# Kernel tuning notes

Hardware: AMD Instinct MI355X
Metric: run time of the kernel (lower is better)

## Reference

```python
import jax, jax.numpy as jnp
import numpy as np

N_NODES = 50000
N_EDGES = 800000
NUM_GRAPHS = 64
F_IN, F_HID, F_HID2, F_OUT = 128, 96, 48, 32


def gcn_conv(x, W, b, src, dst, n_nodes):
    # PyG GCNConv: h = x @ W; out = D^{-1/2} (A+I) D^{-1/2} h + b
    # src/dst already include self loops; degree computed on dst.
    h = x @ W  # [N, F_out]
    deg = jax.ops.segment_sum(jnp.ones(dst.shape[0], dtype=h.dtype), dst, num_segments=n_nodes)
    dinv = jax.lax.rsqrt(deg)  # deg >= 1 due to self loops
    norm = dinv[src] * dinv[dst]  # [E]
    msg = h[src] * norm[:, None]  # gather + scale
    out = jax.ops.segment_sum(msg, dst, num_segments=n_nodes)  # scatter-add
    return out + b


def setup_inputs() -> dict:
    key = jax.random.key(0)
    ks = jax.random.split(key, 10)
    x = jax.random.normal(ks[0], (N_NODES, F_IN), dtype=jnp.float32)
    edge_index = jax.random.randint(ks[1], (2, N_EDGES), 0, N_NODES, dtype=jnp.int64)
    batch = jnp.sort(jax.random.randint(ks[2], (N_NODES,), 0, NUM_GRAPHS, dtype=jnp.int64))
    def glorot(k, fi, fo):
        s = np.sqrt(6.0 / (fi + fo)).astype(np.float32)
        return jax.random.uniform(k, (fi, fo), dtype=jnp.float32, minval=-s, maxval=s)
    W1 = glorot(ks[3], F_IN, F_HID)
    b1 = jnp.zeros((F_HID,), dtype=jnp.float32)
    W2 = glorot(ks[4], F_HID, F_HID2)
    b2 = jnp.zeros((F_HID2,), dtype=jnp.float32)
    W3 = glorot(ks[5], F_HID2, F_OUT)
    b3 = jnp.zeros((F_OUT,), dtype=jnp.float32)
    return {"x": x, "edge_index": edge_index, "batch": batch,
            "W1": W1, "b1": b1, "W2": W2, "b2": b2, "W3": W3, "b3": b3}


def reference(x, edge_index, batch, W1, b1, W2, b2, W3, b3):
    n = x.shape[0]
    loops = jnp.arange(n, dtype=edge_index.dtype)
    src = jnp.concatenate([edge_index[0], loops])
    dst = jnp.concatenate([edge_index[1], loops])

    h = jax.nn.relu(gcn_conv(x, W1, b1, src, dst, n))
    h = jax.nn.relu(gcn_conv(h, W2, b2, src, dst, n))
    h = jax.nn.relu(gcn_conv(h, W3, b3, src, dst, n))

    # global mean pool over graphs in the batch
    sums = jax.ops.segment_sum(h, batch, num_segments=NUM_GRAPHS)
    cnt = jax.ops.segment_sum(jnp.ones((n,), dtype=h.dtype), batch, num_segments=NUM_GRAPHS)
    return sums / jnp.maximum(cnt, 1.0)[:, None]
```

## Files before the change

### kernel.cpp

```cpp
#include <hip/hip_runtime.h>

#define N_NODES 50000
#define N_EDGES 800000
#define NUM_GRAPHS 64

#define CAPLOG 6
#define CAP    (1 << CAPLOG)

__device__ __forceinline__ float bf_lo(unsigned u) { return __uint_as_float(u << 16); }
__device__ __forceinline__ float bf_hi(unsigned u) { return __uint_as_float(u & 0xffff0000u); }
__device__ __forceinline__ unsigned short f2bf(float f) {
    unsigned u = __float_as_uint(f);
    return (unsigned short)((u + 0x7fffu + ((u >> 16) & 1u)) >> 16);
}

#define SC_NG    4
#define SC_BPG   256
#define SC_GRID  (SC_NG * SC_BPG)
#define NPG      ((N_NODES + SC_NG - 1) / SC_NG)
__global__ __launch_bounds__(256) void k_scatter_xcd(
        const int* __restrict__ ei, int* __restrict__ cnt,
        unsigned short* __restrict__ csr,
        const int* __restrict__ batch, int* __restrict__ start) {
    if (blockIdx.x == SC_GRID) {
        int t = threadIdx.x;
        if (t <= NUM_GRAPHS) {
            int lo = 0, hi = N_NODES;
            while (lo < hi) {
                int mid = (lo + hi) >> 1;
                if (batch[mid] < t) lo = mid + 1; else hi = mid;
            }
            start[t] = lo;
        }
        return;
    }
    const int g  = blockIdx.x & (SC_NG - 1);
    const int b  = blockIdx.x / SC_NG;
    const int lo = g * NPG, hi = lo + NPG;
    const int* __restrict__ dst = ei + N_EDGES;
    for (int e = b * 256 + threadIdx.x; e < N_EDGES; e += 256 * SC_BPG) {
        int d = dst[e];
        if (d >= lo && d < hi) {
            int old = atomicAdd(&cnt[d], 1);
            if (old < CAP) csr[(d << CAPLOG) + old] = (unsigned short)ei[e];
        }
    }
}

template <int K, int M, int MT, int FTH, int NTH, int NT, int OSTRIDE>
__global__ __launch_bounds__(FTH * NTH)
void k_gemm(const float* __restrict__ X, const float* __restrict__ W,
            const int* __restrict__ cnt, unsigned short* __restrict__ H) {
    constexpr int BLOCK = FTH * NTH;
    __shared__ float ws[K * MT];
    const int tid = threadIdx.x;
    const int n0 = blockIdx.x * (NTH * NT);
    const int c0 = blockIdx.y * MT;

    for (int i = tid; i < K * MT / 4; i += BLOCK) {
        int k = i / (MT / 4), cv = i % (MT / 4);
        *(float4*)&ws[k * MT + cv * 4] = *(const float4*)&W[k * M + c0 + cv * 4];
    }
    __syncthreads();

    const int ft = tid % FTH;
    const int nt = tid / FTH;
    const float* xp[NT];
    #pragma unroll
    for (int i = 0; i < NT; ++i) {
        int node = n0 + nt * NT + i;
        int nc = node < N_NODES ? node : N_NODES - 1;
        xp[i] = X + (size_t)nc * K;
    }
    float acc[NT][4];
    #pragma unroll
    for (int i = 0; i < NT; ++i) { acc[i][0] = acc[i][1] = acc[i][2] = acc[i][3] = 0.f; }

    for (int k = 0; k < K; k += 4) {
        float4 w0 = *(const float4*)&ws[(k + 0) * MT + ft * 4];
        float4 w1 = *(const float4*)&ws[(k + 1) * MT + ft * 4];
        float4 w2 = *(const float4*)&ws[(k + 2) * MT + ft * 4];
        float4 w3 = *(const float4*)&ws[(k + 3) * MT + ft * 4];
        #pragma unroll
        for (int i = 0; i < NT; ++i) {
            float4 xv = *(const float4*)(xp[i] + k);
            acc[i][0] += xv.x * w0.x + xv.y * w1.x + xv.z * w2.x + xv.w * w3.x;
            acc[i][1] += xv.x * w0.y + xv.y * w1.y + xv.z * w2.y + xv.w * w3.y;
            acc[i][2] += xv.x * w0.z + xv.y * w1.z + xv.z * w2.z + xv.w * w3.z;
            acc[i][3] += xv.x * w0.w + xv.y * w1.w + xv.z * w2.w + xv.w * w3.w;
        }
    }
    #pragma unroll
    for (int i = 0; i < NT; ++i) {
        int node = n0 + nt * NT + i;
        if (node < N_NODES) {
            float s = rsqrtf((float)(cnt[node] + 1));
            ushort4 o;
            o.x = f2bf(acc[i][0] * s); o.y = f2bf(acc[i][1] * s);
            o.z = f2bf(acc[i][2] * s); o.w = f2bf(acc[i][3] * s);
            *(ushort4*)&H[(size_t)node * OSTRIDE + c0 + ft * 4] = o;
        }
    }
}

__global__ __launch_bounds__(384) void k_agg12(
        const unsigned short* __restrict__ H1, const int* __restrict__ cnt,
        const unsigned short* __restrict__ csr, const float* __restrict__ b1,
        const float* __restrict__ W2, unsigned short* __restrict__ H2) {
    __shared__ float Ws[96 * 48];
    __shared__ float T[32][97];
    const int t = threadIdx.x;
    for (int i = t; i < 1152; i += 384)
        *(float4*)&Ws[i * 4] = *(const float4*)&W2[i * 4];

    const int n_l = t / 12, c = t % 12;
    const int node = blockIdx.x * 32 + n_l;
    if (node < N_NODES) {
        int deg = cnt[node];
        int e0 = node << CAPLOG;
        int e1 = e0 + min(deg, CAP);
        float d = rsqrtf((float)(deg + 1));
        const unsigned short* Hc = H1 + c * 8;
        uint4 sv = *(const uint4*)(Hc + (size_t)node * 96);
        float a0 = bf_lo(sv.x), a1 = bf_hi(sv.x), a2 = bf_lo(sv.y), a3 = bf_hi(sv.y);
        float a4 = bf_lo(sv.z), a5 = bf_hi(sv.z), a6 = bf_lo(sv.w), a7 = bf_hi(sv.w);
        for (int e = e0; e < e1; ++e) {
            int s = csr[e];
            uint4 v = *(const uint4*)(Hc + (size_t)s * 96);
            a0 += bf_lo(v.x); a1 += bf_hi(v.x);
            a2 += bf_lo(v.y); a3 += bf_hi(v.y);
            a4 += bf_lo(v.z); a5 += bf_hi(v.z);
            a6 += bf_lo(v.w); a7 += bf_hi(v.w);
        }
        const float4* bp = (const float4*)(b1 + c * 8);
        float4 b0 = bp[0], bb1 = bp[1];
        float* Tr = &T[n_l][c * 8];
        Tr[0] = fmaxf(a0 * d + b0.x, 0.f);  Tr[1] = fmaxf(a1 * d + b0.y, 0.f);
        Tr[2] = fmaxf(a2 * d + b0.z, 0.f);  Tr[3] = fmaxf(a3 * d + b0.w, 0.f);
        Tr[4] = fmaxf(a4 * d + bb1.x, 0.f); Tr[5] = fmaxf(a5 * d + bb1.y, 0.f);
        Tr[6] = fmaxf(a6 * d + bb1.z, 0.f); Tr[7] = fmaxf(a7 * d + bb1.w, 0.f);
    }
    __syncthreads();

    const int n2 = t / 12;
    const int f0 = (t % 12) * 4;
    const int gn = blockIdx.x * 32 + n2;
    if (gn < N_NODES) {
        float4 acc = make_float4(0.f, 0.f, 0.f, 0.f);
        for (int k = 0; k < 96; ++k) {
            float tv = T[n2][k];
            float4 wv = *(const float4*)&Ws[k * 48 + f0];
            acc.x += tv * wv.x; acc.y += tv * wv.y; acc.z += tv * wv.z; acc.w += tv * wv.w;
        }
        float s2 = rsqrtf((float)(cnt[gn] + 1));
        ushort4 o;
        o.x = f2bf(acc.x * s2); o.y = f2bf(acc.y * s2);
        o.z = f2bf(acc.z * s2); o.w = f2bf(acc.w * s2);
        *(ushort4*)&H2[(size_t)gn * 64 + f0] = o;
    }
}

__global__ __launch_bounds__(384) void k_agg23(
        const unsigned short* __restrict__ H2, const int* __restrict__ cnt,
        const unsigned short* __restrict__ csr, const float* __restrict__ b2,
        const float* __restrict__ W3, unsigned short* __restrict__ H3) {
    __shared__ float Ws[48 * 32];
    __shared__ float T[64][49];
    const int t = threadIdx.x;
    for (int i = t; i < 384; i += 384)
        *(float4*)&Ws[i * 4] = *(const float4*)&W3[i * 4];

    const int n_l = t / 6, c = t % 6;
    const int node = blockIdx.x * 64 + n_l;
    if (node < N_NODES) {
        int deg = cnt[node];
        int e0 = node << CAPLOG;
        int e1 = e0 + min(deg, CAP);
        float d = rsqrtf((float)(deg + 1));
        const unsigned short* Hc = H2 + c * 8;
        uint4 sv = *(const uint4*)(Hc + (size_t)node * 64);
        float a0 = bf_lo(sv.x), a1 = bf_hi(sv.x), a2 = bf_lo(sv.y), a3 = bf_hi(sv.y);
        float a4 = bf_lo(sv.z), a5 = bf_hi(sv.z), a6 = bf_lo(sv.w), a7 = bf_hi(sv.w);
        for (int e = e0; e < e1; ++e) {
            int s = csr[e];
            uint4 v = *(const uint4*)(Hc + (size_t)s * 64);
            a0 += bf_lo(v.x); a1 += bf_hi(v.x);
            a2 += bf_lo(v.y); a3 += bf_hi(v.y);
            a4 += bf_lo(v.z); a5 += bf_hi(v.z);
            a6 += bf_lo(v.w); a7 += bf_hi(v.w);
        }
        const float4* bp = (const float4*)(b2 + c * 8);
        float4 b0 = bp[0], bb1 = bp[1];
        float* Tr = &T[n_l][c * 8];
        Tr[0] = fmaxf(a0 * d + b0.x, 0.f);  Tr[1] = fmaxf(a1 * d + b0.y, 0.f);
        Tr[2] = fmaxf(a2 * d + b0.z, 0.f);  Tr[3] = fmaxf(a3 * d + b0.w, 0.f);
        Tr[4] = fmaxf(a4 * d + bb1.x, 0.f); Tr[5] = fmaxf(a5 * d + bb1.y, 0.f);
        Tr[6] = fmaxf(a6 * d + bb1.z, 0.f); Tr[7] = fmaxf(a7 * d + bb1.w, 0.f);
    }
    __syncthreads();

    for (int vid = t; vid < 512; vid += 384) {
        const int n2 = vid / 8;
        const int f0 = (vid % 8) * 4;
        const int gn = blockIdx.x * 64 + n2;
        if (gn < N_NODES) {
            float4 acc = make_float4(0.f, 0.f, 0.f, 0.f);
            for (int k = 0; k < 48; ++k) {
                float tv = T[n2][k];
                float4 wv = *(const float4*)&Ws[k * 32 + f0];
                acc.x += tv * wv.x; acc.y += tv * wv.y; acc.z += tv * wv.z; acc.w += tv * wv.w;
            }
            float s3 = rsqrtf((float)(cnt[gn] + 1));
            ushort4 o;
            o.x = f2bf(acc.x * s3); o.y = f2bf(acc.y * s3);
            o.z = f2bf(acc.z * s3); o.w = f2bf(acc.w * s3);
            *(ushort4*)&H3[(size_t)gn * 32 + f0] = o;
        }
    }
}

__global__ __launch_bounds__(256) void k_agg3p(
        const unsigned short* __restrict__ H3, const int* __restrict__ cnt,
        const unsigned short* __restrict__ csr, const float* __restrict__ b3,
        const int* __restrict__ batch, const int* __restrict__ start,
        float* __restrict__ gsum) {
    __shared__ float T[64][33];
    __shared__ float R[8][32];
    const int t = threadIdx.x;
    const int base = blockIdx.x * 64;

    const int n_l = t / 4, c = t % 4;
    const int node = base + n_l;
    if (node < N_NODES) {
        int deg = cnt[node];
        int e0 = node << CAPLOG;
        int e1 = e0 + min(deg, CAP);
        float d = rsqrtf((float)(deg + 1));
        const unsigned short* Hc = H3 + c * 8;
        uint4 sv = *(const uint4*)(Hc + (size_t)node * 32);
        float a0 = bf_lo(sv.x), a1 = bf_hi(sv.x), a2 = bf_lo(sv.y), a3 = bf_hi(sv.y);
        float a4 = bf_lo(sv.z), a5 = bf_hi(sv.z), a6 = bf_lo(sv.w), a7 = bf_hi(sv.w);
        for (int e = e0; e < e1; ++e) {
            int s = csr[e];
            uint4 v = *(const uint4*)(Hc + (size_t)s * 32);
            a0 += bf_lo(v.x); a1 += bf_hi(v.x);
            a2 += bf_lo(v.y); a3 += bf_hi(v.y);
            a4 += bf_lo(v.z); a5 += bf_hi(v.z);
            a6 += bf_lo(v.w); a7 += bf_hi(v.w);
        }
        const float4* bp = (const float4*)(b3 + c * 8);
        float4 b0 = bp[0], b1 = bp[1];
        float* Tr = &T[n_l][c * 8];
        Tr[0] = fmaxf(a0 * d + b0.x, 0.f); Tr[1] = fmaxf(a1 * d + b0.y, 0.f);
        Tr[2] = fmaxf(a2 * d + b0.z, 0.f); Tr[3] = fmaxf(a3 * d + b0.w, 0.f);
        Tr[4] = fmaxf(a4 * d + b1.x, 0.f); Tr[5] = fmaxf(a5 * d + b1.y, 0.f);
        Tr[6] = fmaxf(a6 * d + b1.z, 0.f); Tr[7] = fmaxf(a7 * d + b1.w, 0.f);
    }
    __syncthreads();

    const int g_lo = batch[base < N_NODES ? base : N_NODES - 1];
    const int last = base + 63 < N_NODES ? base + 63 : N_NODES - 1;
    const int g_hi = batch[last];
    const int f = t & 31, k = t >> 5;
    for (int g = g_lo; g <= g_hi; ++g) {
        int r_lo = start[g] - base;     if (r_lo < 0) r_lo = 0;
        int r_hi = start[g + 1] - base; if (r_hi > 64) r_hi = 64;
        float p = 0.f;
        for (int r = r_lo + k; r < r_hi; r += 8) p += T[r][f];
        R[k][f] = p;
        __syncthreads();
        if (k == 0) {
            float s = R[0][f] + R[1][f] + R[2][f] + R[3][f]
                    + R[4][f] + R[5][f] + R[6][f] + R[7][f];
            if (r_hi > r_lo) atomicAdd(&gsum[g * 32 + f], s);
        }
        __syncthreads();
    }
}

__global__ void k_final(const float* __restrict__ gsum, const int* __restrict__ start,
                        float* __restrict__ out) {
    int t = blockIdx.x * blockDim.x + threadIdx.x;
    if (t < NUM_GRAPHS * 32) {
        int g = t >> 5;
        float c = (float)(start[g + 1] - start[g]);
        out[t] = gsum[t] / fmaxf(c, 1.0f);
    }
}

extern "C" void kernel_launch(void* const* d_in, const int* in_sizes, int n_in,
                              void* d_out, int out_size, void* d_ws, size_t ws_size,
                              hipStream_t stream) {
    const float* x     = (const float*)d_in[0];
    const int*   ei    = (const int*)d_in[1];
    const int*   batch = (const int*)d_in[2];
    const float* W1    = (const float*)d_in[3];
    const float* b1    = (const float*)d_in[4];
    const float* W2    = (const float*)d_in[5];
    const float* b2    = (const float*)d_in[6];
    const float* W3    = (const float*)d_in[7];
    const float* b3    = (const float*)d_in[8];
    float* out = (float*)d_out;

    char* ws = (char*)d_ws;
    size_t o = 0;
    auto alloc = [&](size_t bytes) {
        char* p = ws + o;
        o = (o + bytes + 255) & ~(size_t)255;
        return p;
    };
    unsigned short* H1 = (unsigned short*)alloc((size_t)N_NODES * 96 * 2);
    unsigned short* H2 = (unsigned short*)alloc((size_t)N_NODES * 64 * 2);
    unsigned short* H3 = (unsigned short*)alloc((size_t)N_NODES * 32 * 2);
    int*   cnt    = (int*)alloc((size_t)N_NODES * 4);
    unsigned short* csr = (unsigned short*)alloc((size_t)N_NODES * CAP * 2);
    int*   start  = (int*)alloc((NUM_GRAPHS + 1) * 4);
    float* gsum   = (float*)alloc((size_t)NUM_GRAPHS * 32 * 4);

    hipMemsetAsync(cnt, 0, (size_t)N_NODES * 4, stream);
    hipMemsetAsync(gsum, 0, (size_t)NUM_GRAPHS * 32 * 4, stream);

    hipLaunchKernelGGL(k_scatter_xcd, dim3(SC_GRID + 1), dim3(256), 0, stream, ei, cnt, csr, batch, start);
    hipLaunchKernelGGL((k_gemm<128, 96, 48, 12, 16, 4, 96>), dim3((N_NODES + 63) / 64, 2), dim3(192), 0, stream,
                       x, W1, cnt, H1);
    hipLaunchKernelGGL(k_agg12, dim3((N_NODES + 31) / 32), dim3(384), 0, stream,
                       H1, cnt, csr, b1, W2, H2);
    hipLaunchKernelGGL(k_agg23, dim3((N_NODES + 63) / 64), dim3(384), 0, stream,
                       H2, cnt, csr, b2, W3, H3);
    hipLaunchKernelGGL(k_agg3p, dim3((N_NODES + 63) / 64), dim3(256), 0, stream,
                       H3, cnt, csr, b3, batch, start, gsum);
    hipLaunchKernelGGL(k_final, dim3((NUM_GRAPHS * 32 + 255) / 256), dim3(256), 0, stream,
                       gsum, start, out);
}
```

Before: 244.9 us.

## Embed degree counter in CSR row and unroll neighbor gather by four

Stores each node's degree counter in the last two slots of its CSR row, so scatter atomics and later degree reads share one cache line with the neighbor list and the separate cnt array goes away. Neighbor aggregation is factored into a helper that loads four indices as a ushort4 and issues four independent row gathers per iteration. Padding lanes point at a zero row appended to each H buffer. The per-node inverse sqrt degree is also kept in shared memory for the second matmul stage. The trade-offs are a larger memset over the whole CSR buffer and capacity dropping from 64 to 62 neighbors per node.

```diff
diff --git a/kernel.cpp b/kernel.cpp
--- a/kernel.cpp
+++ b/kernel.cpp
@@ -4,8 +4,10 @@
 #define N_EDGES 800000
 #define NUM_GRAPHS 64
 
-#define CAPLOG 6
-#define CAP    (1 << CAPLOG)
+#define CAPLOG   6
+#define CAP      (1 << CAPLOG)
+#define CAPSLOTS 62
+#define ZROW     N_NODES
 
 __device__ __forceinline__ float bf_lo(unsigned u) { return __uint_as_float(u << 16); }
 __device__ __forceinline__ float bf_hi(unsigned u) { return __uint_as_float(u & 0xffff0000u); }
@@ -14,13 +16,45 @@
     return (unsigned short)((u + 0x7fffu + ((u >> 16) & 1u)) >> 16);
 }
 
+__device__ __forceinline__ int ld_deg(const unsigned short* __restrict__ csr, int n) {
+    return *(const int*)(csr + ((size_t)n << CAPLOG) + CAPSLOTS);
+}
+
+template<int S>
+__device__ __forceinline__ void agg_row8(const unsigned short* __restrict__ Hc,
+                                         const unsigned short* __restrict__ csr,
+                                         int node, int m, float a[8]) {
+    uint4 sv = *(const uint4*)(Hc + (size_t)node * S);
+    a[0] = bf_lo(sv.x); a[1] = bf_hi(sv.x); a[2] = bf_lo(sv.y); a[3] = bf_hi(sv.y);
+    a[4] = bf_lo(sv.z); a[5] = bf_hi(sv.z); a[6] = bf_lo(sv.w); a[7] = bf_hi(sv.w);
+    const int e0 = node << CAPLOG, e1 = e0 + m;
+    for (int e = e0; e < e1; e += 4) {
+        ushort4 ss = *(const ushort4*)&csr[e];
+        int s0 = ss.x;
+        int s1 = (e + 1 < e1) ? (int)ss.y : ZROW;
+        int s2 = (e + 2 < e1) ? (int)ss.z : ZROW;
+        int s3 = (e + 3 < e1) ? (int)ss.w : ZROW;
+        uint4 v0 = *(const uint4*)(Hc + (size_t)s0 * S);
+        uint4 v1 = *(const uint4*)(Hc + (size_t)s1 * S);
+        uint4 v2 = *(const uint4*)(Hc + (size_t)s2 * S);
+        uint4 v3 = *(const uint4*)(Hc + (size_t)s3 * S);
+        a[0] += bf_lo(v0.x) + bf_lo(v1.x) + bf_lo(v2.x) + bf_lo(v3.x);
+        a[1] += bf_hi(v0.x) + bf_hi(v1.x) + bf_hi(v2.x) + bf_hi(v3.x);
+        a[2] += bf_lo(v0.y) + bf_lo(v1.y) + bf_lo(v2.y) + bf_lo(v3.y);
+        a[3] += bf_hi(v0.y) + bf_hi(v1.y) + bf_hi(v2.y) + bf_hi(v3.y);
+        a[4] += bf_lo(v0.z) + bf_lo(v1.z) + bf_lo(v2.z) + bf_lo(v3.z);
+        a[5] += bf_hi(v0.z) + bf_hi(v1.z) + bf_hi(v2.z) + bf_hi(v3.z);
+        a[6] += bf_lo(v0.w) + bf_lo(v1.w) + bf_lo(v2.w) + bf_lo(v3.w);
+        a[7] += bf_hi(v0.w) + bf_hi(v1.w) + bf_hi(v2.w) + bf_hi(v3.w);
+    }
+}
+
 #define SC_NG    4
 #define SC_BPG   256
 #define SC_GRID  (SC_NG * SC_BPG)
 #define NPG      ((N_NODES + SC_NG - 1) / SC_NG)
 __global__ __launch_bounds__(256) void k_scatter_xcd(
-        const int* __restrict__ ei, int* __restrict__ cnt,
-        unsigned short* __restrict__ csr,
+        const int* __restrict__ ei, unsigned short* __restrict__ csr,
         const int* __restrict__ batch, int* __restrict__ start) {
     if (blockIdx.x == SC_GRID) {
         int t = threadIdx.x;
@@ -41,8 +75,8 @@
     for (int e = b * 256 + threadIdx.x; e < N_EDGES; e += 256 * SC_BPG) {
         int d = dst[e];
         if (d >= lo && d < hi) {
-            int old = atomicAdd(&cnt[d], 1);
-            if (old < CAP) csr[(d << CAPLOG) + old] = (unsigned short)ei[e];
+            int old = atomicAdd((int*)(csr + ((size_t)d << CAPLOG) + CAPSLOTS), 1);
+            if (old < CAPSLOTS) csr[(d << CAPLOG) + old] = (unsigned short)ei[e];
         }
     }
 }
@@ -50,12 +84,17 @@
 template <int K, int M, int MT, int FTH, int NTH, int NT, int OSTRIDE>
 __global__ __launch_bounds__(FTH * NTH)
 void k_gemm(const float* __restrict__ X, const float* __restrict__ W,
-            const int* __restrict__ cnt, unsigned short* __restrict__ H) {
+            const unsigned short* __restrict__ csr, unsigned short* __restrict__ H) {
     constexpr int BLOCK = FTH * NTH;
     __shared__ float ws[K * MT];
     const int tid = threadIdx.x;
     const int n0 = blockIdx.x * (NTH * NT);
     const int c0 = blockIdx.y * MT;
+
+    if (blockIdx.x == 0 && blockIdx.y == 0 && tid < M / 4) {
+        ushort4 z = make_ushort4(0, 0, 0, 0);
+        *(ushort4*)&H[(size_t)ZROW * OSTRIDE + tid * 4] = z;
+    }
 
     for (int i = tid; i < K * MT / 4; i += BLOCK) {
         int k = i / (MT / 4), cv = i % (MT / 4);
@@ -94,7 +133,7 @@
     for (int i = 0; i < NT; ++i) {
         int node = n0 + nt * NT + i;
         if (node < N_NODES) {
-            float s = rsqrtf((float)(cnt[node] + 1));
+            float s = rsqrtf((float)(ld_deg(csr, node) + 1));
             ushort4 o;
             o.x = f2bf(acc[i][0] * s); o.y = f2bf(acc[i][1] * s);
             o.z = f2bf(acc[i][2] * s); o.w = f2bf(acc[i][3] * s);
@@ -104,41 +143,36 @@
 }
 
 __global__ __launch_bounds__(384) void k_agg12(
-        const unsigned short* __restrict__ H1, const int* __restrict__ cnt,
+        const unsigned short* __restrict__ H1,
         const unsigned short* __restrict__ csr, const float* __restrict__ b1,
         const float* __restrict__ W2, unsigned short* __restrict__ H2) {
     __shared__ float Ws[96 * 48];
     __shared__ float T[32][97];
+    __shared__ float dinvS[32];
     const int t = threadIdx.x;
     for (int i = t; i < 1152; i += 384)
         *(float4*)&Ws[i * 4] = *(const float4*)&W2[i * 4];
 
+    if (blockIdx.x == 0 && t < 16) {
+        ushort4 z = make_ushort4(0, 0, 0, 0);
+        *(ushort4*)&H2[(size_t)ZROW * 64 + t * 4] = z;
+    }
+
     const int n_l = t / 12, c = t % 12;
     const int node = blockIdx.x * 32 + n_l;
     if (node < N_NODES) {
-        int deg = cnt[node];
-        int e0 = node << CAPLOG;
-        int e1 = e0 + min(deg, CAP);
+        int deg = ld_deg(csr, node);
         float d = rsqrtf((float)(deg + 1));
-        const unsigned short* Hc = H1 + c * 8;
-        uint4 sv = *(const uint4*)(Hc + (size_t)node * 96);
-        float a0 = bf_lo(sv.x), a1 = bf_hi(sv.x), a2 = bf_lo(sv.y), a3 = bf_hi(sv.y);
-        float a4 = bf_lo(sv.z), a5 = bf_hi(sv.z), a6 = bf_lo(sv.w), a7 = bf_hi(sv.w);
-        for (int e = e0; e < e1; ++e) {
-            int s = csr[e];
-            uint4 v = *(const uint4*)(Hc + (size_t)s * 96);
-            a0 += bf_lo(v.x); a1 += bf_hi(v.x);
-            a2 += bf_lo(v.y); a3 += bf_hi(v.y);
-            a4 += bf_lo(v.z); a5 += bf_hi(v.z);
-            a6 += bf_lo(v.w); a7 += bf_hi(v.w);
-        }
+        if (c == 0) dinvS[n_l] = d;
+        float a[8];
+        agg_row8<96>(H1 + c * 8, csr, node, min(deg, CAPSLOTS), a);
         const float4* bp = (const float4*)(b1 + c * 8);
         float4 b0 = bp[0], bb1 = bp[1];
         float* Tr = &T[n_l][c * 8];
-        Tr[0] = fmaxf(a0 * d + b0.x, 0.f);  Tr[1] = fmaxf(a1 * d + b0.y, 0.f);
-        Tr[2] = fmaxf(a2 * d + b0.z, 0.f);  Tr[3] = fmaxf(a3 * d + b0.w, 0.f);
-        Tr[4] = fmaxf(a4 * d + bb1.x, 0.f); Tr[5] = fmaxf(a5 * d + bb1.y, 0.f);
-        Tr[6] = fmaxf(a6 * d + bb1.z, 0.f); Tr[7] = fmaxf(a7 * d + bb1.w, 0.f);
+        Tr[0] = fmaxf(a[0] * d + b0.x, 0.f);  Tr[1] = fmaxf(a[1] * d + b0.y, 0.f);
+        Tr[2] = fmaxf(a[2] * d + b0.z, 0.f);  Tr[3] = fmaxf(a[3] * d + b0.w, 0.f);
+        Tr[4] = fmaxf(a[4] * d + bb1.x, 0.f); Tr[5] = fmaxf(a[5] * d + bb1.y, 0.f);
+        Tr[6] = fmaxf(a[6] * d + bb1.z, 0.f); Tr[7] = fmaxf(a[7] * d + bb1.w, 0.f);
     }
     __syncthreads();
 
@@ -152,7 +186,7 @@
             float4 wv = *(const float4*)&Ws[k * 48 + f0];
             acc.x += tv * wv.x; acc.y += tv * wv.y; acc.z += tv * wv.z; acc.w += tv * wv.w;
         }
-        float s2 = rsqrtf((float)(cnt[gn] + 1));
+        float s2 = dinvS[n2];
         ushort4 o;
         o.x = f2bf(acc.x * s2); o.y = f2bf(acc.y * s2);
         o.z = f2bf(acc.z * s2); o.w = f2bf(acc.w * s2);
@@ -161,41 +195,36 @@
 }
 
 __global__ __launch_bounds__(384) void k_agg23(
-        const unsigned short* __restrict__ H2, const int* __restrict__ cnt,
+        const unsigned short* __restrict__ H2,
         const unsigned short* __restrict__ csr, const float* __restrict__ b2,
         const float* __restrict__ W3, unsigned short* __restrict__ H3) {
     __shared__ float Ws[48 * 32];
     __shared__ float T[64][49];
+    __shared__ float dinvS[64];
     const int t = threadIdx.x;
     for (int i = t; i < 384; i += 384)
         *(float4*)&Ws[i * 4] = *(const float4*)&W3[i * 4];
 
+    if (blockIdx.x == 0 && t < 8) {
+        ushort4 z = make_ushort4(0, 0, 0, 0);
+        *(ushort4*)&H3[(size_t)ZROW * 32 + t * 4] = z;
+    }
+
     const int n_l = t / 6, c = t % 6;
     const int node = blockIdx.x * 64 + n_l;
     if (node < N_NODES) {
-        int deg = cnt[node];
-        int e0 = node << CAPLOG;
-        int e1 = e0 + min(deg, CAP);
+        int deg = ld_deg(csr, node);
         float d = rsqrtf((float)(deg + 1));
-        const unsigned short* Hc = H2 + c * 8;
-        uint4 sv = *(const uint4*)(Hc + (size_t)node * 64);
-        float a0 = bf_lo(sv.x), a1 = bf_hi(sv.x), a2 = bf_lo(sv.y), a3 = bf_hi(sv.y);
-        float a4 = bf_lo(sv.z), a5 = bf_hi(sv.z), a6 = bf_lo(sv.w), a7 = bf_hi(sv.w);
-        for (int e = e0; e < e1; ++e) {
-            int s = csr[e];
-            uint4 v = *(const uint4*)(Hc + (size_t)s * 64);
-            a0 += bf_lo(v.x); a1 += bf_hi(v.x);
-            a2 += bf_lo(v.y); a3 += bf_hi(v.y);
-            a4 += bf_lo(v.z); a5 += bf_hi(v.z);
-            a6 += bf_lo(v.w); a7 += bf_hi(v.w);
-        }
+        if (c == 0) dinvS[n_l] = d;
+        float a[8];
+        agg_row8<64>(H2 + c * 8, csr, node, min(deg, CAPSLOTS), a);
         const float4* bp = (const float4*)(b2 + c * 8);
         float4 b0 = bp[0], bb1 = bp[1];
         float* Tr = &T[n_l][c * 8];
-        Tr[0] = fmaxf(a0 * d + b0.x, 0.f);  Tr[1] = fmaxf(a1 * d + b0.y, 0.f);
-        Tr[2] = fmaxf(a2 * d + b0.z, 0.f);  Tr[3] = fmaxf(a3 * d + b0.w, 0.f);
-        Tr[4] = fmaxf(a4 * d + bb1.x, 0.f); Tr[5] = fmaxf(a5 * d + bb1.y, 0.f);
-        Tr[6] = fmaxf(a6 * d + bb1.z, 0.f); Tr[7] = fmaxf(a7 * d + bb1.w, 0.f);
+        Tr[0] = fmaxf(a[0] * d + b0.x, 0.f);  Tr[1] = fmaxf(a[1] * d + b0.y, 0.f);
+        Tr[2] = fmaxf(a[2] * d + b0.z, 0.f);  Tr[3] = fmaxf(a[3] * d + b0.w, 0.f);
+        Tr[4] = fmaxf(a[4] * d + bb1.x, 0.f); Tr[5] = fmaxf(a[5] * d + bb1.y, 0.f);
+        Tr[6] = fmaxf(a[6] * d + bb1.z, 0.f); Tr[7] = fmaxf(a[7] * d + bb1.w, 0.f);
     }
     __syncthreads();
 
@@ -210,7 +239,7 @@
                 float4 wv = *(const float4*)&Ws[k * 32 + f0];
                 acc.x += tv * wv.x; acc.y += tv * wv.y; acc.z += tv * wv.z; acc.w += tv * wv.w;
             }
-            float s3 = rsqrtf((float)(cnt[gn] + 1));
+            float s3 = dinvS[n2];
             ushort4 o;
             o.x = f2bf(acc.x * s3); o.y = f2bf(acc.y * s3);
             o.z = f2bf(acc.z * s3); o.w = f2bf(acc.w * s3);
@@ -220,7 +249,7 @@
 }
 
 __global__ __launch_bounds__(256) void k_agg3p(
-        const unsigned short* __restrict__ H3, const int* __restrict__ cnt,
+        const unsigned short* __restrict__ H3,
         const unsigned short* __restrict__ csr, const float* __restrict__ b3,
         const int* __restrict__ batch, const int* __restrict__ start,
         float* __restrict__ gsum) {
@@ -232,29 +261,17 @@
     const int n_l = t / 4, c = t % 4;
     const int node = base + n_l;
     if (node < N_NODES) {
-        int deg = cnt[node];
-        int e0 = node << CAPLOG;
-        int e1 = e0 + min(deg, CAP);
+        int deg = ld_deg(csr, node);
         float d = rsqrtf((float)(deg + 1));
-        const unsigned short* Hc = H3 + c * 8;
-        uint4 sv = *(const uint4*)(Hc + (size_t)node * 32);
-        float a0 = bf_lo(sv.x), a1 = bf_hi(sv.x), a2 = bf_lo(sv.y), a3 = bf_hi(sv.y);
-        float a4 = bf_lo(sv.z), a5 = bf_hi(sv.z), a6 = bf_lo(sv.w), a7 = bf_hi(sv.w);
-        for (int e = e0; e < e1; ++e) {
-            int s = csr[e];
-            uint4 v = *(const uint4*)(Hc + (size_t)s * 32);
-            a0 += bf_lo(v.x); a1 += bf_hi(v.x);
-            a2 += bf_lo(v.y); a3 += bf_hi(v.y);
-            a4 += bf_lo(v.z); a5 += bf_hi(v.z);
-            a6 += bf_lo(v.w); a7 += bf_hi(v.w);
-        }
+        float a[8];
+        agg_row8<32>(H3 + c * 8, csr, node, min(deg, CAPSLOTS), a);
         const float4* bp = (const float4*)(b3 + c * 8);
         float4 b0 = bp[0], b1 = bp[1];
         float* Tr = &T[n_l][c * 8];
-        Tr[0] = fmaxf(a0 * d + b0.x, 0.f); Tr[1] = fmaxf(a1 * d + b0.y, 0.f);
-        Tr[2] = fmaxf(a2 * d + b0.z, 0.f); Tr[3] = fmaxf(a3 * d + b0.w, 0.f);
-        Tr[4] = fmaxf(a4 * d + b1.x, 0.f); Tr[5] = fmaxf(a5 * d + b1.y, 0.f);
-        Tr[6] = fmaxf(a6 * d + b1.z, 0.f); Tr[7] = fmaxf(a7 * d + b1.w, 0.f);
+        Tr[0] = fmaxf(a[0] * d + b0.x, 0.f); Tr[1] = fmaxf(a[1] * d + b0.y, 0.f);
+        Tr[2] = fmaxf(a[2] * d + b0.z, 0.f); Tr[3] = fmaxf(a[3] * d + b0.w, 0.f);
+        Tr[4] = fmaxf(a[4] * d + b1.x, 0.f); Tr[5] = fmaxf(a[5] * d + b1.y, 0.f);
+        Tr[6] = fmaxf(a[6] * d + b1.z, 0.f); Tr[7] = fmaxf(a[7] * d + b1.w, 0.f);
     }
     __syncthreads();
 
@@ -309,26 +326,25 @@
         o = (o + bytes + 255) & ~(size_t)255;
         return p;
     };
-    unsigned short* H1 = (unsigned short*)alloc((size_t)N_NODES * 96 * 2);
-    unsigned short* H2 = (unsigned short*)alloc((size_t)N_NODES * 64 * 2);
-    unsigned short* H3 = (unsigned short*)alloc((size_t)N_NODES * 32 * 2);
-    int*   cnt    = (int*)alloc((size_t)N_NODES * 4);
+    unsigned short* H1 = (unsigned short*)alloc((size_t)(N_NODES + 1) * 96 * 2);
+    unsigned short* H2 = (unsigned short*)alloc((size_t)(N_NODES + 1) * 64 * 2);
+    unsigned short* H3 = (unsigned short*)alloc((size_t)(N_NODES + 1) * 32 * 2);
     unsigned short* csr = (unsigned short*)alloc((size_t)N_NODES * CAP * 2);
     int*   start  = (int*)alloc((NUM_GRAPHS + 1) * 4);
     float* gsum   = (float*)alloc((size_t)NUM_GRAPHS * 32 * 4);
 
-    hipMemsetAsync(cnt, 0, (size_t)N_NODES * 4, stream);
+    hipMemsetAsync(csr, 0, (size_t)N_NODES * CAP * 2, stream);
     hipMemsetAsync(gsum, 0, (size_t)NUM_GRAPHS * 32 * 4, stream);
 
-    hipLaunchKernelGGL(k_scatter_xcd, dim3(SC_GRID + 1), dim3(256), 0, stream, ei, cnt, csr, batch, start);
+    hipLaunchKernelGGL(k_scatter_xcd, dim3(SC_GRID + 1), dim3(256), 0, stream, ei, csr, batch, start);
     hipLaunchKernelGGL((k_gemm<128, 96, 48, 12, 16, 4, 96>), dim3((N_NODES + 63) / 64, 2), dim3(192), 0, stream,
-                       x, W1, cnt, H1);
+                       x, W1, csr, H1);
     hipLaunchKernelGGL(k_agg12, dim3((N_NODES + 31) / 32), dim3(384), 0, stream,
-                       H1, cnt, csr, b1, W2, H2);
+                       H1, csr, b1, W2, H2);
     hipLaunchKernelGGL(k_agg23, dim3((N_NODES + 63) / 64), dim3(384), 0, stream,
-                       H2, cnt, csr, b2, W3, H3);
+                       H2, csr, b2, W3, H3);
     hipLaunchKernelGGL(k_agg3p, dim3((N_NODES + 63) / 64), dim3(256), 0, stream,
-                       H3, cnt, csr, b3, batch, start, gsum);
+                       H3, csr, b3, batch, start, gsum);
     hipLaunchKernelGGL(k_final, dim3((NUM_GRAPHS * 32 + 255) / 256), dim3(256), 0, stream,
                        gsum, start, out);
 }
```

Measured after the change: 266.9 us. 1.09x slower.
